# Performance work log

Measured on AMD Instinct MI355X. Metric: run time of the kernel, lower is better.

Reference implementation:

```python
import jax, jax.numpy as jnp
import numpy as np

N = 100000      # nodes
E = 1600000     # edges
F_IN = 64       # num_features
H = 64          # nhid
G = 512         # num graphs in batch
C = 2           # num_classes
BN_EPS = 1e-5


def setup_inputs() -> dict:
    key = jax.random.key(0)
    ks = jax.random.split(key, 8)
    x = jax.random.normal(ks[0], (N, F_IN), jnp.float32)
    edge_index = jax.random.randint(ks[1], (2, E), 0, N, dtype=jnp.int64)
    batch = jnp.sort(jax.random.randint(ks[2], (N,), 0, G, dtype=jnp.int64))
    s = lambda k, shp, fan: (jax.random.normal(k, shp, jnp.float32) / np.sqrt(fan)).astype(jnp.float32)
    W1 = s(ks[3], (F_IN, H), F_IN); b1 = jnp.zeros((H,), jnp.float32)
    W2 = s(ks[4], (H, H), H);       b2 = jnp.zeros((H,), jnp.float32)
    Wg = s(ks[5], (H, 1), H);       bg = jnp.zeros((1,), jnp.float32)
    bn_gamma = jnp.ones((H,), jnp.float32); bn_beta = jnp.zeros((H,), jnp.float32)
    bn_mean = jnp.zeros((H,), jnp.float32); bn_var = jnp.ones((H,), jnp.float32)
    W_lin = s(ks[6], (H, C), H);    b_lin = jnp.zeros((C,), jnp.float32)
    return dict(x=x, edge_index=edge_index, batch=batch,
                W1=W1, b1=b1, W2=W2, b2=b2, Wg=Wg, bg=bg,
                bn_gamma=bn_gamma, bn_beta=bn_beta, bn_mean=bn_mean, bn_var=bn_var,
                W_lin=W_lin, b_lin=b_lin)


def reference(x, edge_index, batch, W1, b1, W2, b2, Wg, bg,
              bn_gamma, bn_beta, bn_mean, bn_var, W_lin, b_lin):
    src, dst = edge_index[0], edge_index[1]
    # GINConv (eps=0): h_i = MLP(x_i + sum_{j->i} x_j)
    agg = jax.ops.segment_sum(x[src], dst, num_segments=N)       # [N, F_IN]
    h = x + agg
    h = jnp.maximum(h @ W1 + b1, 0.0) @ W2 + b2                  # [N, H]
    h = jnp.maximum(h, 0.0)                                      # outer ReLU
    # Attentional aggregation: segment softmax of gate, weighted segment-sum
    gate = (h @ Wg + bg)[:, 0]                                   # [N]
    gmax = jax.ops.segment_max(gate, batch, num_segments=G)      # [G]
    ex = jnp.exp(gate - gmax[batch])                             # [N]
    denom = jax.ops.segment_sum(ex, batch, num_segments=G)       # [G]
    alpha = ex / denom[batch]                                    # [N]
    pooled = jax.ops.segment_sum(alpha[:, None] * h, batch, num_segments=G)  # [G, H]
    # BatchNorm1d in eval mode (running stats); dropout is identity in eval
    norm = (pooled - bn_mean) / jnp.sqrt(bn_var + BN_EPS) * bn_gamma + bn_beta
    logits = norm @ W_lin + b_lin                                # [G, C]
    return jax.nn.log_softmax(logits, axis=-1)
```

## Files before the change

### kernel.cpp

```cpp
#include <hip/hip_runtime.h>
#include <math.h>
#include <float.h>

#define BN_EPS 1e-5f
#define PBLK   2048
#define NBUCKP 832
#define ACAP   4096

typedef short s16x8 __attribute__((ext_vector_type(8)));
typedef float f32x4 __attribute__((ext_vector_type(4)));

__device__ __forceinline__ unsigned short f2bf(float f) {
    unsigned u = __float_as_uint(f);
    u += 0x7FFFu + ((u >> 16) & 1u);
    return (unsigned short)(u >> 16);
}
__device__ __forceinline__ float bf2f(unsigned short b) {
    return __uint_as_float(((unsigned)b) << 16);
}
__device__ __forceinline__ int vtb(int row, int byteoff) {
    return row * 128 + (byteoff ^ ((row & 7) << 4));
}

__global__ __launch_bounds__(512) void prep_partition(
    const float* __restrict__ x, unsigned short* __restrict__ xb,
    const float* __restrict__ W1, const float* __restrict__ W2,
    unsigned short* __restrict__ w1t, unsigned short* __restrict__ w2t,
    const int* __restrict__ src, const int* __restrict__ dst,
    const int* __restrict__ batch, int* __restrict__ gstart,
    int* __restrict__ bcur0, int* __restrict__ packed2,
    int N, int E, int EB, int G)
{
    __shared__ int hist[NBUCKP], lstart[NBUCKP], goff[NBUCKP], cur[NBUCKP];

    int tid = threadIdx.x;
    int lane = tid & 63;
    int blk = blockIdx.x;

    int n4 = N * 16;
    for (int i = blk * 512 + tid; i < n4; i += gridDim.x * 512) {
        float4 f = *(const float4*)(x + (size_t)i * 4);
        ushort4 o;
        o.x = f2bf(f.x); o.y = f2bf(f.y); o.z = f2bf(f.z); o.w = f2bf(f.w);
        *(ushort4*)(xb + (size_t)i * 4) = o;
    }
    for (int i = blk * 512 + tid; i < N; i += gridDim.x * 512) {
        int bi = batch[i];
        int bp = (i == 0) ? -1 : batch[i - 1];
        for (int g = bp + 1; g <= bi; ++g) gstart[g] = i;
        if (i == N - 1)
            for (int g = bi + 1; g <= G; ++g) gstart[g] = N;
    }
    if (blk == 0)
        for (int idx = tid; idx < 4096; idx += 512)
            w1t[idx] = f2bf(W1[(idx & 63) * 64 + (idx >> 6)]);
    if (blk == 1)
        for (int idx = tid; idx < 4096; idx += 512)
            w2t[idx] = f2bf(W2[(idx & 63) * 64 + (idx >> 6)]);

    if (blk >= EB) return;

    int e0 = blk * PBLK;
    int cnt = E - e0; if (cnt > PBLK) cnt = PBLK; if (cnt < 0) cnt = 0;

    for (int i = tid; i < NBUCKP; i += 512) hist[i] = 0;
    __syncthreads();
    for (int i = tid; i < cnt; i += 512)
        atomicAdd(&hist[dst[e0 + i] >> 7], 1);
    __syncthreads();
    if (tid < 64) {
        int carry = 0;
        #pragma unroll
        for (int c = 0; c < NBUCKP / 64; ++c) {
            int idx = c * 64 + lane;
            int v = hist[idx];
            int xv = v;
            #pragma unroll
            for (int d = 1; d < 64; d <<= 1) {
                int t = __shfl_up(xv, d); if (lane >= d) xv += t;
            }
            lstart[idx] = xv - v + carry;
            cur[idx]    = xv - v + carry;
            carry += __shfl(xv, 63);
        }
    }
    __syncthreads();
    for (int i = tid; i < NBUCKP; i += 512)
        if (hist[i] > 0) goff[i] = atomicAdd(&bcur0[i], hist[i]);
    __syncthreads();
    for (int i = tid; i < cnt; i += 512) {
        int d = dst[e0 + i];
        int s = src[e0 + i];
        int b = d >> 7;
        int p = atomicAdd(&cur[b], 1);
        packed2[(size_t)b * ACAP + goff[b] + (p - lstart[b])] = ((d & 127) << 17) | s;
    }
}

__global__ __launch_bounds__(512) void bucket_fused(
    const unsigned short* __restrict__ xb,
    int* __restrict__ packed2, const int* __restrict__ bcur0,
    const unsigned short* __restrict__ w1t, const unsigned short* __restrict__ w2t,
    const float* __restrict__ b1, const float* __restrict__ b2,
    const float* __restrict__ Wg, const float* __restrict__ bg,
    unsigned short* __restrict__ h_out, float* __restrict__ gate_out, int N)
{
    __shared__ char vt_raw[16384];
    int* hist = (int*)vt_raw;
    int* cur  = hist + 128;
    int* excl = (int*)(vt_raw + 1024);

    int tid = threadIdx.x;
    int lane = tid & 63;
    int wave = tid >> 6;
    int b = blockIdx.x;
    int node0 = b * 128;
    int ecnt = bcur0[b];
    if (ecnt > ACAP) ecnt = ACAP;
    int* arena = packed2 + (size_t)b * ACAP;

    if (tid < 128) hist[tid] = 0;
    __syncthreads();

    int ev[8];
    #pragma unroll
    for (int k = 0; k < 8; ++k) {
        int i = tid + k * 512;
        int val = -1;
        if (i < ecnt) {
            val = arena[i];
            atomicAdd(&hist[val >> 17], 1);
        }
        ev[k] = val;
    }
    __syncthreads();

    if (tid < 64) {
        int carry = 0;
        #pragma unroll
        for (int c = 0; c < 2; ++c) {
            int idx = c * 64 + lane;
            int v = hist[idx];
            int xv = v;
            #pragma unroll
            for (int d = 1; d < 64; d <<= 1) {
                int t = __shfl_up(xv, d); if (lane >= d) xv += t;
            }
            excl[idx] = xv - v + carry;
            cur[idx]  = xv - v + carry;
            carry += __shfl(xv, 63);
        }
        if (lane == 0) excl[128] = carry;
    }
    __syncthreads();

    #pragma unroll
    for (int k = 0; k < 8; ++k) {
        int val = ev[k];
        if (val >= 0) {
            int p = atomicAdd(&cur[val >> 17], 1);
            arena[p] = val & 0x1FFFF;
        }
    }
    __syncthreads();

    int rowbase = wave * 16;
    int exv = excl[rowbase + (lane < 17 ? lane : 16)];
    __syncthreads();

    {
        int beg  = __builtin_amdgcn_readlane(exv, 0);
        int end_ = __builtin_amdgcn_readlane(exv, 1);
        int ei   = (beg + lane < end_) ? arena[beg + lane] : 0;

        for (int m = 0; m < 16; ++m) {
            int cbeg = beg, cend = end_, cei = ei;
            if (m < 15) {
                beg  = end_;
                end_ = __builtin_amdgcn_readlane(exv, m + 2);
                ei   = (beg + lane < end_) ? arena[beg + lane] : 0;
            }
            int ln = rowbase + m;
            int node = node0 + ln;
            if (node < N) {
                float v0 = bf2f(xb[(size_t)node * 64 + lane]);
                float v1 = 0.f, v2 = 0.f, v3 = 0.f, v4 = 0.f, v5 = 0.f, v6 = 0.f, v7 = 0.f;

                int eiv = cei;
                for (int base = cbeg; base < cend; base += 64) {
                    if (base != cbeg)
                        eiv = (base + lane < cend) ? arena[base + lane] : 0;
                    int cnt = cend - base; if (cnt > 64) cnt = 64;
                    int j = 0;
                    for (; j + 8 <= cnt; j += 8) {
                        int s0 = __builtin_amdgcn_readlane(eiv, j + 0);
                        int s1 = __builtin_amdgcn_readlane(eiv, j + 1);
                        int s2 = __builtin_amdgcn_readlane(eiv, j + 2);
                        int s3 = __builtin_amdgcn_readlane(eiv, j + 3);
                        int s4 = __builtin_amdgcn_readlane(eiv, j + 4);
                        int s5 = __builtin_amdgcn_readlane(eiv, j + 5);
                        int s6 = __builtin_amdgcn_readlane(eiv, j + 6);
                        int s7 = __builtin_amdgcn_readlane(eiv, j + 7);
                        unsigned short t0 = xb[(size_t)s0 * 64 + lane];
                        unsigned short t1 = xb[(size_t)s1 * 64 + lane];
                        unsigned short t2 = xb[(size_t)s2 * 64 + lane];
                        unsigned short t3 = xb[(size_t)s3 * 64 + lane];
                        unsigned short t4 = xb[(size_t)s4 * 64 + lane];
                        unsigned short t5 = xb[(size_t)s5 * 64 + lane];
                        unsigned short t6 = xb[(size_t)s6 * 64 + lane];
                        unsigned short t7 = xb[(size_t)s7 * 64 + lane];
                        v0 += bf2f(t0); v1 += bf2f(t1); v2 += bf2f(t2); v3 += bf2f(t3);
                        v4 += bf2f(t4); v5 += bf2f(t5); v6 += bf2f(t6); v7 += bf2f(t7);
                    }
                    for (; j + 4 <= cnt; j += 4) {
                        int s0 = __builtin_amdgcn_readlane(eiv, j + 0);
                        int s1 = __builtin_amdgcn_readlane(eiv, j + 1);
                        int s2 = __builtin_amdgcn_readlane(eiv, j + 2);
                        int s3 = __builtin_amdgcn_readlane(eiv, j + 3);
                        unsigned short t0 = xb[(size_t)s0 * 64 + lane];
                        unsigned short t1 = xb[(size_t)s1 * 64 + lane];
                        unsigned short t2 = xb[(size_t)s2 * 64 + lane];
                        unsigned short t3 = xb[(size_t)s3 * 64 + lane];
                        v4 += bf2f(t0); v5 += bf2f(t1); v6 += bf2f(t2); v7 += bf2f(t3);
                    }
                    for (; j < cnt; ++j) {
                        int s = __builtin_amdgcn_readlane(eiv, j);
                        v1 += bf2f(xb[(size_t)s * 64 + lane]);
                    }
                }
                float v = ((v0 + v1) + (v2 + v3)) + ((v4 + v5) + (v6 + v7));
                *(unsigned short*)(vt_raw + vtb(ln, lane * 2)) = f2bf(v);
            } else {
                *(unsigned short*)(vt_raw + vtb(ln, lane * 2)) = 0;
            }
        }
    }

    {
        int quad = lane >> 4;
        int col  = lane & 15;

        s16x8 a0 = *(const s16x8*)(vt_raw + vtb(rowbase + col, quad * 16));
        s16x8 a1 = *(const s16x8*)(vt_raw + vtb(rowbase + col, 64 + quad * 16));

        float b1v[4], b2v[4], wgv[4];
        #pragma unroll
        for (int nt = 0; nt < 4; ++nt) {
            b1v[nt] = b1[nt * 16 + col];
            b2v[nt] = b2[nt * 16 + col];
            wgv[nt] = Wg[nt * 16 + col];
        }
        float bgv = bg[0];

        f32x4 acc1[4];
        #pragma unroll
        for (int nt = 0; nt < 4; ++nt) {
            int off = (nt * 16 + col) * 64 + quad * 8;
            s16x8 w0 = *(const s16x8*)(w1t + off);
            s16x8 w1 = *(const s16x8*)(w1t + off + 32);
            f32x4 c = {0.f, 0.f, 0.f, 0.f};
            c = __builtin_amdgcn_mfma_f32_16x16x32_bf16(a0, w0, c, 0, 0, 0);
            c = __builtin_amdgcn_mfma_f32_16x16x32_bf16(a1, w1, c, 0, 0, 0);
            acc1[nt] = c;
        }
        #pragma unroll
        for (int nt = 0; nt < 4; ++nt)
            #pragma unroll
            for (int r = 0; r < 4; ++r) {
                float hv = fmaxf(acc1[nt][r] + b1v[nt], 0.f);
                *(unsigned short*)(vt_raw + vtb(rowbase + quad * 4 + r, (nt * 16 + col) * 2)) = f2bf(hv);
            }

        s16x8 g0 = *(const s16x8*)(vt_raw + vtb(rowbase + col, quad * 16));
        s16x8 g1 = *(const s16x8*)(vt_raw + vtb(rowbase + col, 64 + quad * 16));

        f32x4 acc2[4];
        #pragma unroll
        for (int nt = 0; nt < 4; ++nt) {
            int off = (nt * 16 + col) * 64 + quad * 8;
            s16x8 w0 = *(const s16x8*)(w2t + off);
            s16x8 w1 = *(const s16x8*)(w2t + off + 32);
            f32x4 c = {0.f, 0.f, 0.f, 0.f};
            c = __builtin_amdgcn_mfma_f32_16x16x32_bf16(g0, w0, c, 0, 0, 0);
            c = __builtin_amdgcn_mfma_f32_16x16x32_bf16(g1, w1, c, 0, 0, 0);
            acc2[nt] = c;
        }

        int nbase = node0 + rowbase;
        float gp[4] = {0.f, 0.f, 0.f, 0.f};
        #pragma unroll
        for (int nt = 0; nt < 4; ++nt)
            #pragma unroll
            for (int r = 0; r < 4; ++r) {
                float hv = fmaxf(acc2[nt][r] + b2v[nt], 0.f);
                int node = nbase + quad * 4 + r;
                if (node < N)
                    h_out[(size_t)node * 64 + nt * 16 + col] = f2bf(hv);
                gp[r] = fmaf(hv, wgv[nt], gp[r]);
            }
        #pragma unroll
        for (int r = 0; r < 4; ++r) {
            float t = gp[r];
            t += __shfl_xor(t, 1);
            t += __shfl_xor(t, 2);
            t += __shfl_xor(t, 4);
            t += __shfl_xor(t, 8);
            int node = nbase + quad * 4 + r;
            if (col == 0 && node < N) gate_out[node] = t + bgv;
        }
    }
}

__global__ __launch_bounds__(256) void pool_final(
    const unsigned short* __restrict__ h, const float* __restrict__ gate,
    const int* __restrict__ gstart,
    const float* __restrict__ gamma_, const float* __restrict__ beta_,
    const float* __restrict__ mean_, const float* __restrict__ var_,
    const float* __restrict__ Wl, const float* __restrict__ bl,
    float* __restrict__ out)
{
    int g = blockIdx.x;
    int tid = threadIdx.x;

    int start = gstart[g];
    int end   = gstart[g + 1];

    __shared__ float red[4];
    __shared__ float pool_s[4 * 64];

    int lane = tid & 63;
    int wave = tid >> 6;

    float m = -FLT_MAX;
    for (int i = start + tid; i < end; i += 256) m = fmaxf(m, gate[i]);
    #pragma unroll
    for (int off = 32; off; off >>= 1) m = fmaxf(m, __shfl_xor(m, off));
    if (lane == 0) red[wave] = m;
    __syncthreads();
    m = fmaxf(fmaxf(red[0], red[1]), fmaxf(red[2], red[3]));
    __syncthreads();

    float s = 0.f;
    for (int i = start + tid; i < end; i += 256) s += expf(gate[i] - m);
    #pragma unroll
    for (int off = 32; off; off >>= 1) s += __shfl_xor(s, off);
    if (lane == 0) red[wave] = s;
    __syncthreads();
    s = red[0] + red[1] + red[2] + red[3];

    float a0 = 0.f, a1 = 0.f, a2 = 0.f, a3 = 0.f;
    int i = start + wave;
    for (; i + 12 < end; i += 16) {
        float e0 = expf(gate[i]      - m);
        float e1 = expf(gate[i + 4]  - m);
        float e2 = expf(gate[i + 8]  - m);
        float e3 = expf(gate[i + 12] - m);
        float t0 = bf2f(h[(size_t)(i)      * 64 + lane]);
        float t1 = bf2f(h[(size_t)(i + 4)  * 64 + lane]);
        float t2 = bf2f(h[(size_t)(i + 8)  * 64 + lane]);
        float t3 = bf2f(h[(size_t)(i + 12) * 64 + lane]);
        a0 = fmaf(e0, t0, a0);
        a1 = fmaf(e1, t1, a1);
        a2 = fmaf(e2, t2, a2);
        a3 = fmaf(e3, t3, a3);
    }
    for (; i < end; i += 4) {
        float e = expf(gate[i] - m);
        a0 = fmaf(e, bf2f(h[(size_t)i * 64 + lane]), a0);
    }
    pool_s[wave * 64 + lane] = (a0 + a1) + (a2 + a3);
    __syncthreads();

    if (wave == 0) {
        float p = pool_s[lane] + pool_s[64 + lane] + pool_s[128 + lane] + pool_s[192 + lane];
        p = (end > start) ? (p / s) : 0.f;
        float nrm = (p - mean_[lane]) / sqrtf(var_[lane] + BN_EPS) * gamma_[lane] + beta_[lane];
        float l0 = nrm * Wl[lane * 2 + 0];
        float l1 = nrm * Wl[lane * 2 + 1];
        #pragma unroll
        for (int off = 32; off; off >>= 1) {
            l0 += __shfl_xor(l0, off);
            l1 += __shfl_xor(l1, off);
        }
        if (lane == 0) {
            l0 += bl[0];
            l1 += bl[1];
            float mx = fmaxf(l0, l1);
            float lse = mx + logf(expf(l0 - mx) + expf(l1 - mx));
            out[g * 2 + 0] = l0 - lse;
            out[g * 2 + 1] = l1 - lse;
        }
    }
}

extern "C" void kernel_launch(void* const* d_in, const int* in_sizes, int n_in,
                              void* d_out, int out_size, void* d_ws, size_t ws_size,
                              hipStream_t stream)
{
    const float* x     = (const float*)d_in[0];
    const int*   eidx  = (const int*)d_in[1];
    const int*   batch = (const int*)d_in[2];
    const float* W1    = (const float*)d_in[3];
    const float* b1    = (const float*)d_in[4];
    const float* W2    = (const float*)d_in[5];
    const float* b2    = (const float*)d_in[6];
    const float* Wg    = (const float*)d_in[7];
    const float* bg    = (const float*)d_in[8];
    const float* bng   = (const float*)d_in[9];
    const float* bnb   = (const float*)d_in[10];
    const float* bnm   = (const float*)d_in[11];
    const float* bnv   = (const float*)d_in[12];
    const float* Wl    = (const float*)d_in[13];
    const float* bl    = (const float*)d_in[14];
    float* out = (float*)d_out;

    int N = in_sizes[0] / 64;
    int E = in_sizes[1] / 2;
    int G = out_size / 2;
    int NP = ((N + 63) / 64) * 64;
    int NBUCK = (N + 127) / 128;
    int EB = (E + PBLK - 1) / PBLK;
    int GRID_A = 1024 > EB ? 1024 : EB;

    char* w = (char*)d_ws;
    int* packed2 = (int*)w;                     w += (size_t)NBUCK * ACAP * 4;
    unsigned short* hxb  = (unsigned short*)w;  w += (size_t)NP * 64 * 2;
    float* gate  = (float*)w;                   w += ((size_t)N * 4 + 255) / 256 * 256;
    int* bcur0   = (int*)w;                     w += NBUCKP * 4;
    unsigned short* w1t = (unsigned short*)w;   w += 4096 * 2;
    unsigned short* w2t = (unsigned short*)w;   w += 4096 * 2;
    int* gstart  = (int*)w;                     w += ((size_t)(G + 1) * 4 + 255) / 256 * 256;
    unsigned short* hbuf = (unsigned short*)w;

    const int* src = eidx;
    const int* dst = eidx + E;

    hipMemsetAsync(bcur0, 0, NBUCKP * sizeof(int), stream);

    prep_partition<<<GRID_A, 512, 0, stream>>>(x, hxb, W1, W2, w1t, w2t,
                                               src, dst, batch, gstart,
                                               bcur0, packed2,
                                               N, E, EB, G);

    bucket_fused  <<<NBUCK, 512, 0, stream>>>(hxb, packed2, bcur0, w1t, w2t,
                                              b1, b2, Wg, bg, hbuf, gate, N);

    pool_final    <<<G, 256, 0, stream>>>(hbuf, gate, gstart, bng, bnb, bnm, bnv,
                                          Wl, bl, out);
}
```

Before: 205.3 us.

## Stage bucket sort in LDS and coalesce global edge writes

```diff
diff --git a/kernel.cpp b/kernel.cpp
--- a/kernel.cpp
+++ b/kernel.cpp
@@ -3,9 +3,10 @@
 #include <float.h>
 
 #define BN_EPS 1e-5f
-#define PBLK   2048
+#define PBLK   8192
 #define NBUCKP 832
 #define ACAP   4096
+#define STCAP  3072
 
 typedef short s16x8 __attribute__((ext_vector_type(8)));
 typedef float f32x4 __attribute__((ext_vector_type(4)));
@@ -32,6 +33,8 @@
     int N, int E, int EB, int G)
 {
     __shared__ int hist[NBUCKP], lstart[NBUCKP], goff[NBUCKP], cur[NBUCKP];
+    __shared__ int sorted[PBLK];
+    __shared__ unsigned short sbkt[PBLK];
 
     int tid = threadIdx.x;
     int lane = tid & 63;
@@ -80,32 +83,40 @@
                 int t = __shfl_up(xv, d); if (lane >= d) xv += t;
             }
             lstart[idx] = xv - v + carry;
-            cur[idx]    = xv - v + carry;
             carry += __shfl(xv, 63);
         }
     }
     __syncthreads();
-    for (int i = tid; i < NBUCKP; i += 512)
+    for (int i = tid; i < NBUCKP; i += 512) {
+        cur[i] = lstart[i];
         if (hist[i] > 0) goff[i] = atomicAdd(&bcur0[i], hist[i]);
+    }
     __syncthreads();
     for (int i = tid; i < cnt; i += 512) {
         int d = dst[e0 + i];
         int s = src[e0 + i];
         int b = d >> 7;
         int p = atomicAdd(&cur[b], 1);
-        packed2[(size_t)b * ACAP + goff[b] + (p - lstart[b])] = ((d & 127) << 17) | s;
-    }
-}
-
-__global__ __launch_bounds__(512) void bucket_fused(
+        sorted[p] = ((d & 127) << 17) | s;
+        sbkt[p] = (unsigned short)b;
+    }
+    __syncthreads();
+    for (int i = tid; i < cnt; i += 512) {
+        int b = sbkt[i];
+        packed2[(size_t)b * ACAP + goff[b] + (i - lstart[b])] = sorted[i];
+    }
+}
+
+__global__ __launch_bounds__(512, 4) void bucket_fused(
     const unsigned short* __restrict__ xb,
-    int* __restrict__ packed2, const int* __restrict__ bcur0,
+    const int* __restrict__ packed2, const int* __restrict__ bcur0,
     const unsigned short* __restrict__ w1t, const unsigned short* __restrict__ w2t,
     const float* __restrict__ b1, const float* __restrict__ b2,
     const float* __restrict__ Wg, const float* __restrict__ bg,
     unsigned short* __restrict__ h_out, float* __restrict__ gate_out, int N)
 {
     __shared__ char vt_raw[16384];
+    __shared__ int stage[STCAP];
     int* hist = (int*)vt_raw;
     int* cur  = hist + 128;
     int* excl = (int*)(vt_raw + 1024);
@@ -117,22 +128,12 @@
     int node0 = b * 128;
     int ecnt = bcur0[b];
     if (ecnt > ACAP) ecnt = ACAP;
-    int* arena = packed2 + (size_t)b * ACAP;
+    const int* arena = packed2 + (size_t)b * ACAP;
 
     if (tid < 128) hist[tid] = 0;
     __syncthreads();
-
-    int ev[8];
-    #pragma unroll
-    for (int k = 0; k < 8; ++k) {
-        int i = tid + k * 512;
-        int val = -1;
-        if (i < ecnt) {
-            val = arena[i];
-            atomicAdd(&hist[val >> 17], 1);
-        }
-        ev[k] = val;
-    }
+    for (int i = tid; i < ecnt; i += 512)
+        atomicAdd(&hist[arena[i] >> 17], 1);
     __syncthreads();
 
     if (tid < 64) {
@@ -154,85 +155,110 @@
     }
     __syncthreads();
 
-    #pragma unroll
-    for (int k = 0; k < 8; ++k) {
-        int val = ev[k];
-        if (val >= 0) {
-            int p = atomicAdd(&cur[val >> 17], 1);
-            arena[p] = val & 0x1FFFF;
-        }
+    for (int i = tid; i < ecnt; i += 512) {
+        int v = arena[i];
+        int p = atomicAdd(&cur[v >> 17], 1);
+        if (p < STCAP) stage[p] = v & 0x1FFFF;
     }
     __syncthreads();
 
     int rowbase = wave * 16;
     int exv = excl[rowbase + (lane < 17 ? lane : 16)];
-    __syncthreads();
-
-    {
-        int beg  = __builtin_amdgcn_readlane(exv, 0);
-        int end_ = __builtin_amdgcn_readlane(exv, 1);
-        int ei   = (beg + lane < end_) ? arena[beg + lane] : 0;
-
-        for (int m = 0; m < 16; ++m) {
-            int cbeg = beg, cend = end_, cei = ei;
-            if (m < 15) {
-                beg  = end_;
-                end_ = __builtin_amdgcn_readlane(exv, m + 2);
-                ei   = (beg + lane < end_) ? arena[beg + lane] : 0;
+    if (exv > STCAP) exv = STCAP;
+    __syncthreads();
+
+    for (int m = 0; m < 16; ++m) {
+        int ln = rowbase + m;
+        int node = node0 + ln;
+        if (node < N) {
+            int beg  = __builtin_amdgcn_readlane(exv, m);
+            int end_ = __builtin_amdgcn_readlane(exv, m + 1);
+
+            float v0 = bf2f(xb[(unsigned)node * 64u + lane]);
+            float v1 = 0.f, v2 = 0.f, v3 = 0.f, v4 = 0.f, v5 = 0.f, v6 = 0.f, v7 = 0.f;
+
+            for (int base = beg; base < end_; base += 64) {
+                int eiv = (base + lane < end_) ? stage[base + lane] : 0;
+                int cnt = end_ - base; if (cnt > 64) cnt = 64;
+                int j = 0;
+                for (; j + 16 <= cnt; j += 16) {
+                    int s0  = __builtin_amdgcn_readlane(eiv, j + 0);
+                    int s1  = __builtin_amdgcn_readlane(eiv, j + 1);
+                    int s2  = __builtin_amdgcn_readlane(eiv, j + 2);
+                    int s3  = __builtin_amdgcn_readlane(eiv, j + 3);
+                    int s4  = __builtin_amdgcn_readlane(eiv, j + 4);
+                    int s5  = __builtin_amdgcn_readlane(eiv, j + 5);
+                    int s6  = __builtin_amdgcn_readlane(eiv, j + 6);
+                    int s7  = __builtin_amdgcn_readlane(eiv, j + 7);
+                    int s8  = __builtin_amdgcn_readlane(eiv, j + 8);
+                    int s9  = __builtin_amdgcn_readlane(eiv, j + 9);
+                    int s10 = __builtin_amdgcn_readlane(eiv, j + 10);
+                    int s11 = __builtin_amdgcn_readlane(eiv, j + 11);
+                    int s12 = __builtin_amdgcn_readlane(eiv, j + 12);
+                    int s13 = __builtin_amdgcn_readlane(eiv, j + 13);
+                    int s14 = __builtin_amdgcn_readlane(eiv, j + 14);
+                    int s15 = __builtin_amdgcn_readlane(eiv, j + 15);
+                    unsigned short t0  = xb[(unsigned)s0  * 64u + lane];
+                    unsigned short t1  = xb[(unsigned)s1  * 64u + lane];
+                    unsigned short t2  = xb[(unsigned)s2  * 64u + lane];
+                    unsigned short t3  = xb[(unsigned)s3  * 64u + lane];
+                    unsigned short t4  = xb[(unsigned)s4  * 64u + lane];
+                    unsigned short t5  = xb[(unsigned)s5  * 64u + lane];
+                    unsigned short t6  = xb[(unsigned)s6  * 64u + lane];
+                    unsigned short t7  = xb[(unsigned)s7  * 64u + lane];
+                    unsigned short t8  = xb[(unsigned)s8  * 64u + lane];
+                    unsigned short t9  = xb[(unsigned)s9  * 64u + lane];
+                    unsigned short t10 = xb[(unsigned)s10 * 64u + lane];
+                    unsigned short t11 = xb[(unsigned)s11 * 64u + lane];
+                    unsigned short t12 = xb[(unsigned)s12 * 64u + lane];
+                    unsigned short t13 = xb[(unsigned)s13 * 64u + lane];
+                    unsigned short t14 = xb[(unsigned)s14 * 64u + lane];
+                    unsigned short t15 = xb[(unsigned)s15 * 64u + lane];
+                    v0 += bf2f(t0); v1 += bf2f(t1); v2 += bf2f(t2); v3 += bf2f(t3);
+                    v4 += bf2f(t4); v5 += bf2f(t5); v6 += bf2f(t6); v7 += bf2f(t7);
+                    v0 += bf2f(t8); v1 += bf2f(t9); v2 += bf2f(t10); v3 += bf2f(t11);
+                    v4 += bf2f(t12); v5 += bf2f(t13); v6 += bf2f(t14); v7 += bf2f(t15);
+                }
+                for (; j + 8 <= cnt; j += 8) {
+                    int s0 = __builtin_amdgcn_readlane(eiv, j + 0);
+                    int s1 = __builtin_amdgcn_readlane(eiv, j + 1);
+                    int s2 = __builtin_amdgcn_readlane(eiv, j + 2);
+                    int s3 = __builtin_amdgcn_readlane(eiv, j + 3);
+                    int s4 = __builtin_amdgcn_readlane(eiv, j + 4);
+                    int s5 = __builtin_amdgcn_readlane(eiv, j + 5);
+                    int s6 = __builtin_amdgcn_readlane(eiv, j + 6);
+                    int s7 = __builtin_amdgcn_readlane(eiv, j + 7);
+                    unsigned short t0 = xb[(unsigned)s0 * 64u + lane];
+                    unsigned short t1 = xb[(unsigned)s1 * 64u + lane];
+                    unsigned short t2 = xb[(unsigned)s2 * 64u + lane];
+                    unsigned short t3 = xb[(unsigned)s3 * 64u + lane];
+                    unsigned short t4 = xb[(unsigned)s4 * 64u + lane];
+                    unsigned short t5 = xb[(unsigned)s5 * 64u + lane];
+                    unsigned short t6 = xb[(unsigned)s6 * 64u + lane];
+                    unsigned short t7 = xb[(unsigned)s7 * 64u + lane];
+                    v0 += bf2f(t0); v1 += bf2f(t1); v2 += bf2f(t2); v3 += bf2f(t3);
+                    v4 += bf2f(t4); v5 += bf2f(t5); v6 += bf2f(t6); v7 += bf2f(t7);
+                }
+                for (; j + 4 <= cnt; j += 4) {
+                    int s0 = __builtin_amdgcn_readlane(eiv, j + 0);
+                    int s1 = __builtin_amdgcn_readlane(eiv, j + 1);
+                    int s2 = __builtin_amdgcn_readlane(eiv, j + 2);
+                    int s3 = __builtin_amdgcn_readlane(eiv, j + 3);
+                    unsigned short t0 = xb[(unsigned)s0 * 64u + lane];
+                    unsigned short t1 = xb[(unsigned)s1 * 64u + lane];
+                    unsigned short t2 = xb[(unsigned)s2 * 64u + lane];
+                    unsigned short t3 = xb[(unsigned)s3 * 64u + lane];
+                    v4 += bf2f(t0); v5 += bf2f(t1); v6 += bf2f(t2); v7 += bf2f(t3);
+                }
+                for (; j < cnt; ++j) {
+                    int s = __builtin_amdgcn_readlane(eiv, j);
+                    v1 += bf2f(xb[(unsigned)s * 64u + lane]);
+                }
             }
-            int ln = rowbase + m;
-            int node = node0 + ln;
-            if (node < N) {
-                float v0 = bf2f(xb[(size_t)node * 64 + lane]);
-                float v1 = 0.f, v2 = 0.f, v3 = 0.f, v4 = 0.f, v5 = 0.f, v6 = 0.f, v7 = 0.f;
-
-                int eiv = cei;
-                for (int base = cbeg; base < cend; base += 64) {
-                    if (base != cbeg)
-                        eiv = (base + lane < cend) ? arena[base + lane] : 0;
-                    int cnt = cend - base; if (cnt > 64) cnt = 64;
-                    int j = 0;
-                    for (; j + 8 <= cnt; j += 8) {
-                        int s0 = __builtin_amdgcn_readlane(eiv, j + 0);
-                        int s1 = __builtin_amdgcn_readlane(eiv, j + 1);
-                        int s2 = __builtin_amdgcn_readlane(eiv, j + 2);
-                        int s3 = __builtin_amdgcn_readlane(eiv, j + 3);
-                        int s4 = __builtin_amdgcn_readlane(eiv, j + 4);
-                        int s5 = __builtin_amdgcn_readlane(eiv, j + 5);
-                        int s6 = __builtin_amdgcn_readlane(eiv, j + 6);
-                        int s7 = __builtin_amdgcn_readlane(eiv, j + 7);
-                        unsigned short t0 = xb[(size_t)s0 * 64 + lane];
-                        unsigned short t1 = xb[(size_t)s1 * 64 + lane];
-                        unsigned short t2 = xb[(size_t)s2 * 64 + lane];
-                        unsigned short t3 = xb[(size_t)s3 * 64 + lane];
-                        unsigned short t4 = xb[(size_t)s4 * 64 + lane];
-                        unsigned short t5 = xb[(size_t)s5 * 64 + lane];
-                        unsigned short t6 = xb[(size_t)s6 * 64 + lane];
-                        unsigned short t7 = xb[(size_t)s7 * 64 + lane];
-                        v0 += bf2f(t0); v1 += bf2f(t1); v2 += bf2f(t2); v3 += bf2f(t3);
-                        v4 += bf2f(t4); v5 += bf2f(t5); v6 += bf2f(t6); v7 += bf2f(t7);
-                    }
-                    for (; j + 4 <= cnt; j += 4) {
-                        int s0 = __builtin_amdgcn_readlane(eiv, j + 0);
-                        int s1 = __builtin_amdgcn_readlane(eiv, j + 1);
-                        int s2 = __builtin_amdgcn_readlane(eiv, j + 2);
-                        int s3 = __builtin_amdgcn_readlane(eiv, j + 3);
-                        unsigned short t0 = xb[(size_t)s0 * 64 + lane];
-                        unsigned short t1 = xb[(size_t)s1 * 64 + lane];
-                        unsigned short t2 = xb[(size_t)s2 * 64 + lane];
-                        unsigned short t3 = xb[(size_t)s3 * 64 + lane];
-                        v4 += bf2f(t0); v5 += bf2f(t1); v6 += bf2f(t2); v7 += bf2f(t3);
-                    }
-                    for (; j < cnt; ++j) {
-                        int s = __builtin_amdgcn_readlane(eiv, j);
-                        v1 += bf2f(xb[(size_t)s * 64 + lane]);
-                    }
-                }
-                float v = ((v0 + v1) + (v2 + v3)) + ((v4 + v5) + (v6 + v7));
-                *(unsigned short*)(vt_raw + vtb(ln, lane * 2)) = f2bf(v);
-            } else {
-                *(unsigned short*)(vt_raw + vtb(ln, lane * 2)) = 0;
-            }
+            float v = ((v0 + v1) + (v2 + v3)) + ((v4 + v5) + (v6 + v7));
+            *(unsigned short*)(vt_raw + vtb(ln, lane * 2)) = f2bf(v);
+        } else {
+            *(unsigned short*)(vt_raw + vtb(ln, lane * 2)) = 0;
         }
     }
 
```

Result: faster. 187.0 us (-8.9%).

## Gather fp32 x directly, drop bf16 copy, use global atomics partition and LDS edge staging

Applied to the files above, without the earlier changes.

```diff
diff --git a/kernel.cpp b/kernel.cpp
--- a/kernel.cpp
+++ b/kernel.cpp
@@ -3,9 +3,9 @@
 #include <float.h>
 
 #define BN_EPS 1e-5f
-#define PBLK   2048
 #define NBUCKP 832
 #define ACAP   4096
+#define STCAP  3072
 
 typedef short s16x8 __attribute__((ext_vector_type(8)));
 typedef float f32x4 __attribute__((ext_vector_type(4)));
@@ -23,28 +23,19 @@
 }
 
 __global__ __launch_bounds__(512) void prep_partition(
-    const float* __restrict__ x, unsigned short* __restrict__ xb,
     const float* __restrict__ W1, const float* __restrict__ W2,
     unsigned short* __restrict__ w1t, unsigned short* __restrict__ w2t,
     const int* __restrict__ src, const int* __restrict__ dst,
     const int* __restrict__ batch, int* __restrict__ gstart,
     int* __restrict__ bcur0, int* __restrict__ packed2,
-    int N, int E, int EB, int G)
+    int N, int E, int G)
 {
-    __shared__ int hist[NBUCKP], lstart[NBUCKP], goff[NBUCKP], cur[NBUCKP];
-
     int tid = threadIdx.x;
-    int lane = tid & 63;
     int blk = blockIdx.x;
-
-    int n4 = N * 16;
-    for (int i = blk * 512 + tid; i < n4; i += gridDim.x * 512) {
-        float4 f = *(const float4*)(x + (size_t)i * 4);
-        ushort4 o;
-        o.x = f2bf(f.x); o.y = f2bf(f.y); o.z = f2bf(f.z); o.w = f2bf(f.w);
-        *(ushort4*)(xb + (size_t)i * 4) = o;
-    }
-    for (int i = blk * 512 + tid; i < N; i += gridDim.x * 512) {
+    int gid = blk * 512 + tid;
+    int stride = gridDim.x * 512;
+
+    for (int i = gid; i < N; i += stride) {
         int bi = batch[i];
         int bp = (i == 0) ? -1 : batch[i - 1];
         for (int g = bp + 1; g <= bi; ++g) gstart[g] = i;
@@ -58,54 +49,26 @@
         for (int idx = tid; idx < 4096; idx += 512)
             w2t[idx] = f2bf(W2[(idx & 63) * 64 + (idx >> 6)]);
 
-    if (blk >= EB) return;
-
-    int e0 = blk * PBLK;
-    int cnt = E - e0; if (cnt > PBLK) cnt = PBLK; if (cnt < 0) cnt = 0;
-
-    for (int i = tid; i < NBUCKP; i += 512) hist[i] = 0;
-    __syncthreads();
-    for (int i = tid; i < cnt; i += 512)
-        atomicAdd(&hist[dst[e0 + i] >> 7], 1);
-    __syncthreads();
-    if (tid < 64) {
-        int carry = 0;
-        #pragma unroll
-        for (int c = 0; c < NBUCKP / 64; ++c) {
-            int idx = c * 64 + lane;
-            int v = hist[idx];
-            int xv = v;
-            #pragma unroll
-            for (int d = 1; d < 64; d <<= 1) {
-                int t = __shfl_up(xv, d); if (lane >= d) xv += t;
-            }
-            lstart[idx] = xv - v + carry;
-            cur[idx]    = xv - v + carry;
-            carry += __shfl(xv, 63);
-        }
-    }
-    __syncthreads();
-    for (int i = tid; i < NBUCKP; i += 512)
-        if (hist[i] > 0) goff[i] = atomicAdd(&bcur0[i], hist[i]);
-    __syncthreads();
-    for (int i = tid; i < cnt; i += 512) {
-        int d = dst[e0 + i];
-        int s = src[e0 + i];
+    for (int i = gid; i < E; i += stride) {
+        int d = dst[i];
+        int s = src[i];
         int b = d >> 7;
-        int p = atomicAdd(&cur[b], 1);
-        packed2[(size_t)b * ACAP + goff[b] + (p - lstart[b])] = ((d & 127) << 17) | s;
+        int p = atomicAdd(&bcur0[b], 1);
+        if (p < ACAP)
+            packed2[(size_t)b * ACAP + p] = ((d & 127) << 17) | s;
     }
 }
 
 __global__ __launch_bounds__(512) void bucket_fused(
-    const unsigned short* __restrict__ xb,
-    int* __restrict__ packed2, const int* __restrict__ bcur0,
+    const float* __restrict__ x,
+    const int* __restrict__ packed2, const int* __restrict__ bcur0,
     const unsigned short* __restrict__ w1t, const unsigned short* __restrict__ w2t,
     const float* __restrict__ b1, const float* __restrict__ b2,
     const float* __restrict__ Wg, const float* __restrict__ bg,
     unsigned short* __restrict__ h_out, float* __restrict__ gate_out, int N)
 {
     __shared__ char vt_raw[16384];
+    __shared__ int stage[STCAP + 64];
     int* hist = (int*)vt_raw;
     int* cur  = hist + 128;
     int* excl = (int*)(vt_raw + 1024);
@@ -117,22 +80,12 @@
     int node0 = b * 128;
     int ecnt = bcur0[b];
     if (ecnt > ACAP) ecnt = ACAP;
-    int* arena = packed2 + (size_t)b * ACAP;
+    const int* arena = packed2 + (size_t)b * ACAP;
 
     if (tid < 128) hist[tid] = 0;
     __syncthreads();
-
-    int ev[8];
-    #pragma unroll
-    for (int k = 0; k < 8; ++k) {
-        int i = tid + k * 512;
-        int val = -1;
-        if (i < ecnt) {
-            val = arena[i];
-            atomicAdd(&hist[val >> 17], 1);
-        }
-        ev[k] = val;
-    }
+    for (int i = tid; i < ecnt; i += 512)
+        atomicAdd(&hist[arena[i] >> 17], 1);
     __syncthreads();
 
     if (tid < 64) {
@@ -154,84 +107,69 @@
     }
     __syncthreads();
 
-    #pragma unroll
-    for (int k = 0; k < 8; ++k) {
-        int val = ev[k];
-        if (val >= 0) {
-            int p = atomicAdd(&cur[val >> 17], 1);
-            arena[p] = val & 0x1FFFF;
-        }
+    for (int i = tid; i < ecnt; i += 512) {
+        int v = arena[i];
+        int p = atomicAdd(&cur[v >> 17], 1);
+        if (p < STCAP) stage[p] = v & 0x1FFFF;
     }
     __syncthreads();
 
     int rowbase = wave * 16;
     int exv = excl[rowbase + (lane < 17 ? lane : 16)];
-    __syncthreads();
-
-    {
-        int beg  = __builtin_amdgcn_readlane(exv, 0);
-        int end_ = __builtin_amdgcn_readlane(exv, 1);
-        int ei   = (beg + lane < end_) ? arena[beg + lane] : 0;
-
-        for (int m = 0; m < 16; ++m) {
-            int cbeg = beg, cend = end_, cei = ei;
-            if (m < 15) {
-                beg  = end_;
-                end_ = __builtin_amdgcn_readlane(exv, m + 2);
-                ei   = (beg + lane < end_) ? arena[beg + lane] : 0;
-            }
-            int ln = rowbase + m;
-            int node = node0 + ln;
-            if (node < N) {
-                float v0 = bf2f(xb[(size_t)node * 64 + lane]);
-                float v1 = 0.f, v2 = 0.f, v3 = 0.f, v4 = 0.f, v5 = 0.f, v6 = 0.f, v7 = 0.f;
-
-                int eiv = cei;
-                for (int base = cbeg; base < cend; base += 64) {
-                    if (base != cbeg)
-                        eiv = (base + lane < cend) ? arena[base + lane] : 0;
-                    int cnt = cend - base; if (cnt > 64) cnt = 64;
-                    int j = 0;
-                    for (; j + 8 <= cnt; j += 8) {
-                        int s0 = __builtin_amdgcn_readlane(eiv, j + 0);
-                        int s1 = __builtin_amdgcn_readlane(eiv, j + 1);
-                        int s2 = __builtin_amdgcn_readlane(eiv, j + 2);
-                        int s3 = __builtin_amdgcn_readlane(eiv, j + 3);
-                        int s4 = __builtin_amdgcn_readlane(eiv, j + 4);
-                        int s5 = __builtin_amdgcn_readlane(eiv, j + 5);
-                        int s6 = __builtin_amdgcn_readlane(eiv, j + 6);
-                        int s7 = __builtin_amdgcn_readlane(eiv, j + 7);
-                        unsigned short t0 = xb[(size_t)s0 * 64 + lane];
-                        unsigned short t1 = xb[(size_t)s1 * 64 + lane];
-                        unsigned short t2 = xb[(size_t)s2 * 64 + lane];
-                        unsigned short t3 = xb[(size_t)s3 * 64 + lane];
-                        unsigned short t4 = xb[(size_t)s4 * 64 + lane];
-                        unsigned short t5 = xb[(size_t)s5 * 64 + lane];
-                        unsigned short t6 = xb[(size_t)s6 * 64 + lane];
-                        unsigned short t7 = xb[(size_t)s7 * 64 + lane];
-                        v0 += bf2f(t0); v1 += bf2f(t1); v2 += bf2f(t2); v3 += bf2f(t3);
-                        v4 += bf2f(t4); v5 += bf2f(t5); v6 += bf2f(t6); v7 += bf2f(t7);
-                    }
-                    for (; j + 4 <= cnt; j += 4) {
-                        int s0 = __builtin_amdgcn_readlane(eiv, j + 0);
-                        int s1 = __builtin_amdgcn_readlane(eiv, j + 1);
-                        int s2 = __builtin_amdgcn_readlane(eiv, j + 2);
-                        int s3 = __builtin_amdgcn_readlane(eiv, j + 3);
-                        unsigned short t0 = xb[(size_t)s0 * 64 + lane];
-                        unsigned short t1 = xb[(size_t)s1 * 64 + lane];
-                        unsigned short t2 = xb[(size_t)s2 * 64 + lane];
-                        unsigned short t3 = xb[(size_t)s3 * 64 + lane];
-                        v4 += bf2f(t0); v5 += bf2f(t1); v6 += bf2f(t2); v7 += bf2f(t3);
-                    }
-                    for (; j < cnt; ++j) {
-                        int s = __builtin_amdgcn_readlane(eiv, j);
-                        v1 += bf2f(xb[(size_t)s * 64 + lane]);
-                    }
+    if (exv > STCAP) exv = STCAP;
+    __syncthreads();
+
+    int q = lane >> 4;
+    int c = lane & 15;
+    unsigned chunk_off = (unsigned)c * 16u;
+    const char* xB = (const char*)x;
+
+    for (int m = 0; m < 16; ++m) {
+        int ln = rowbase + m;
+        int node = node0 + ln;
+        if (node < N) {
+            int beg  = __builtin_amdgcn_readlane(exv, m);
+            int end_ = __builtin_amdgcn_readlane(exv, m + 1);
+
+            float a0 = 0.f, a1 = 0.f, a2 = 0.f, a3 = 0.f;
+
+            for (int base = beg; base < end_; base += 64) {
+                int eiv = stage[base + lane];
+                int deg = end_ - base; if (deg > 64) deg = 64;
+                int kfull = deg >> 2;
+                int idx = q * 4;
+                for (int k = 0; k < kfull; ++k) {
+                    int s = __builtin_amdgcn_ds_bpermute(idx, eiv);
+                    f32x4 f = *(const f32x4*)(xB + ((unsigned)s * 256u + chunk_off));
+                    a0 += f[0]; a1 += f[1]; a2 += f[2]; a3 += f[3];
+                    idx += 16;
                 }
-                float v = ((v0 + v1) + (v2 + v3)) + ((v4 + v5) + (v6 + v7));
-                *(unsigned short*)(vt_raw + vtb(ln, lane * 2)) = f2bf(v);
-            } else {
-                *(unsigned short*)(vt_raw + vtb(ln, lane * 2)) = 0;
+                if (deg & 3) {
+                    int e = (kfull << 2) + q;
+                    int ec = (e < deg) ? e : (deg - 1);
+                    int s = __builtin_amdgcn_ds_bpermute(ec << 2, eiv);
+                    float msk = (e < deg) ? 1.f : 0.f;
+                    f32x4 f = *(const f32x4*)(xB + ((unsigned)s * 256u + chunk_off));
+                    a0 = fmaf(f[0], msk, a0); a1 = fmaf(f[1], msk, a1);
+                    a2 = fmaf(f[2], msk, a2); a3 = fmaf(f[3], msk, a3);
+                }
+            }
+            a0 += __shfl_xor(a0, 16); a1 += __shfl_xor(a1, 16);
+            a2 += __shfl_xor(a2, 16); a3 += __shfl_xor(a3, 16);
+            a0 += __shfl_xor(a0, 32); a1 += __shfl_xor(a1, 32);
+            a2 += __shfl_xor(a2, 32); a3 += __shfl_xor(a3, 32);
+            f32x4 sf = *(const f32x4*)(xB + ((unsigned)node * 256u + chunk_off));
+            a0 += sf[0]; a1 += sf[1]; a2 += sf[2]; a3 += sf[3];
+            if (q == 0) {
+                unsigned lo = (unsigned)f2bf(a0) | ((unsigned)f2bf(a1) << 16);
+                unsigned hi = (unsigned)f2bf(a2) | ((unsigned)f2bf(a3) << 16);
+                uint2 pk = {lo, hi};
+                *(uint2*)(vt_raw + vtb(ln, c * 8)) = pk;
+            }
+        } else {
+            if (q == 0) {
+                uint2 z = {0u, 0u};
+                *(uint2*)(vt_raw + vtb(ln, c * 8)) = z;
             }
         }
     }
@@ -258,10 +196,10 @@
             int off = (nt * 16 + col) * 64 + quad * 8;
             s16x8 w0 = *(const s16x8*)(w1t + off);
             s16x8 w1 = *(const s16x8*)(w1t + off + 32);
-            f32x4 c = {0.f, 0.f, 0.f, 0.f};
-            c = __builtin_amdgcn_mfma_f32_16x16x32_bf16(a0, w0, c, 0, 0, 0);
-            c = __builtin_amdgcn_mfma_f32_16x16x32_bf16(a1, w1, c, 0, 0, 0);
-            acc1[nt] = c;
+            f32x4 cc = {0.f, 0.f, 0.f, 0.f};
+            cc = __builtin_amdgcn_mfma_f32_16x16x32_bf16(a0, w0, cc, 0, 0, 0);
+            cc = __builtin_amdgcn_mfma_f32_16x16x32_bf16(a1, w1, cc, 0, 0, 0);
+            acc1[nt] = cc;
         }
         #pragma unroll
         for (int nt = 0; nt < 4; ++nt)
@@ -280,10 +218,10 @@
             int off = (nt * 16 + col) * 64 + quad * 8;
             s16x8 w0 = *(const s16x8*)(w2t + off);
             s16x8 w1 = *(const s16x8*)(w2t + off + 32);
-            f32x4 c = {0.f, 0.f, 0.f, 0.f};
-            c = __builtin_amdgcn_mfma_f32_16x16x32_bf16(g0, w0, c, 0, 0, 0);
-            c = __builtin_amdgcn_mfma_f32_16x16x32_bf16(g1, w1, c, 0, 0, 0);
-            acc2[nt] = c;
+            f32x4 cc = {0.f, 0.f, 0.f, 0.f};
+            cc = __builtin_amdgcn_mfma_f32_16x16x32_bf16(g0, w0, cc, 0, 0, 0);
+            cc = __builtin_amdgcn_mfma_f32_16x16x32_bf16(g1, w1, cc, 0, 0, 0);
+            acc2[nt] = cc;
         }
 
         int nbase = node0 + rowbase;
@@ -417,14 +355,10 @@
     int N = in_sizes[0] / 64;
     int E = in_sizes[1] / 2;
     int G = out_size / 2;
-    int NP = ((N + 63) / 64) * 64;
     int NBUCK = (N + 127) / 128;
-    int EB = (E + PBLK - 1) / PBLK;
-    int GRID_A = 1024 > EB ? 1024 : EB;
 
     char* w = (char*)d_ws;
     int* packed2 = (int*)w;                     w += (size_t)NBUCK * ACAP * 4;
-    unsigned short* hxb  = (unsigned short*)w;  w += (size_t)NP * 64 * 2;
     float* gate  = (float*)w;                   w += ((size_t)N * 4 + 255) / 256 * 256;
     int* bcur0   = (int*)w;                     w += NBUCKP * 4;
     unsigned short* w1t = (unsigned short*)w;   w += 4096 * 2;
@@ -437,12 +371,12 @@
 
     hipMemsetAsync(bcur0, 0, NBUCKP * sizeof(int), stream);
 
-    prep_partition<<<GRID_A, 512, 0, stream>>>(x, hxb, W1, W2, w1t, w2t,
-                                               src, dst, batch, gstart,
-                                               bcur0, packed2,
-                                               N, E, EB, G);
-
-    bucket_fused  <<<NBUCK, 512, 0, stream>>>(hxb, packed2, bcur0, w1t, w2t,
+    prep_partition<<<1024, 512, 0, stream>>>(W1, W2, w1t, w2t,
+                                             src, dst, batch, gstart,
+                                             bcur0, packed2,
+                                             N, E, G);
+
+    bucket_fused  <<<NBUCK, 512, 0, stream>>>(x, packed2, bcur0, w1t, w2t,
                                               b1, b2, Wg, bg, hbuf, gate, N);
 
     pool_final    <<<G, 256, 0, stream>>>(hbuf, gate, gstart, bng, bnb, bnm, bnv,
```

New measurement: 556.0 us. 171% more time.
